# Optimization experiments

Measured on AMD Instinct MI355X. Metric: run time of the kernel, lower is better.

The kernel has to match this reference:

```python
import jax, jax.numpy as jnp
import numpy as np

E, L, D, H, S, B = 8, 12, 768, 12, 512, 32
DIMS = [12, 8, 8, 8, 8, 12]
RANKS = [1, 8, 8, 8, 8, 8, 1]
ALPHA = 8.0


def setup_inputs() -> dict:
    key = jax.random.key(0)
    ks = iter(jax.random.split(key, 32))
    inp = {}
    inp['hidden_states'] = jax.random.normal(next(ks), (B, S, D), jnp.float32)
    inp['router_weights'] = jax.random.normal(next(ks), (D, E), jnp.float32)
    for pre in ('q', 'v'):
        for i in range(6):
            shp = (E, L, RANKS[i], DIMS[i], RANKS[i + 1])
            inp[f'{pre}_core{i}'] = jax.random.normal(next(ks), shp, jnp.float32) * 0.05
    for nm in ('Wq', 'Wk', 'Wv', 'Wo'):
        inp[nm] = jax.random.normal(next(ks), (L, D, D), jnp.float32) * 0.02
    for nm in ('bq', 'bk', 'bv', 'bo'):
        inp[nm] = jnp.zeros((L, D), jnp.float32)
    inp['ln_scale'] = jnp.ones((L, D), jnp.float32)
    inp['ln_bias'] = jnp.zeros((L, D), jnp.float32)
    return inp


def _layernorm(x, scale, bias, eps=1e-12):
    mu = x.mean(-1, keepdims=True)
    var = ((x - mu) ** 2).mean(-1, keepdims=True)
    return (x - mu) * jax.lax.rsqrt(var + eps) * scale + bias


def _tt_weights(cores):
    # cores[i]: [L, r_i, d_i, r_{i+1}]; chained TT contraction, vectorized over layers
    w = jnp.einsum('Lijk,Lklm,Lmno,Lopq,Lqrs,Lstu->Ljlnprt', *cores)
    return w.reshape(w.shape[0], D, D)  # [L, out, in] (matches torch weight.reshape)


def reference(hidden_states, router_weights,
              q_core0, q_core1, q_core2, q_core3, q_core4, q_core5,
              v_core0, v_core1, v_core2, v_core3, v_core4, v_core5,
              Wq, Wk, Wv, Wo, bq, bk, bv, bo, ln_scale, ln_bias):
    # routing: pool over sequence, softmax + argmax per sample
    pooled = hidden_states.mean(axis=1)                      # [B, D]
    probs = jax.nn.softmax(pooled @ router_weights, axis=-1)  # [B, E]
    idx = jnp.argmax(probs, axis=-1)                          # [B]
    e = idx[-1]
    qc = [c[e] for c in (q_core0, q_core1, q_core2, q_core3, q_core4, q_core5)]
    vc = [c[e] for c in (v_core0, v_core1, v_core2, v_core3, v_core4, v_core5)]
    Wq_a = Wq + ALPHA * _tt_weights(qc)  # [L, D, D]
    Wv_a = Wv + ALPHA * _tt_weights(vc)

    hd = D // H
    scale = 1.0 / jnp.sqrt(jnp.float32(hd))
    x = hidden_states
    for l in range(L):
        q = (x @ Wq_a[l].T + bq[l]).reshape(B, S, H, hd)
        k = (x @ Wk[l].T + bk[l]).reshape(B, S, H, hd)
        v = (x @ Wv_a[l].T + bv[l]).reshape(B, S, H, hd)
        scores = jnp.einsum('bqhd,bkhd->bhqk', q, k) * scale
        attn = jax.nn.softmax(scores, axis=-1)
        ctx = jnp.einsum('bhqk,bkhd->bqhd', attn, v).reshape(B, S, D)
        out = ctx @ Wo[l].T + bo[l]
        x = _layernorm(x + out, ln_scale[l], ln_bias[l])
    return x
```

## Files before the change

### kernel.cpp

```cpp
#include <hip/hip_runtime.h>
#include <hip/hip_bf16.h>
#include <stdint.h>

#define E_ 8
#define L_ 12
#define D_ 768
#define H_ 12
#define S_ 512
#define B_ 32
#define BS_ (B_*S_)

typedef __attribute__((ext_vector_type(4))) float floatx4;
typedef __attribute__((ext_vector_type(8))) __bf16 bf16x8;
typedef __attribute__((ext_vector_type(4))) __bf16 bf16x4;
typedef __attribute__((ext_vector_type(2))) unsigned uintx2;

__device__ __forceinline__ __bf16 f2bf(float f) {
  unsigned u = __builtin_bit_cast(unsigned, f);
  u += 0x7fffu + ((u >> 16) & 1u);
  unsigned short h = (unsigned short)(u >> 16);
  return __builtin_bit_cast(__bf16, h);
}

__device__ __forceinline__ unsigned cvtpk_bf16(float lo, float hi) {
  unsigned r;
  asm("v_cvt_pk_bf16_f32 %0, %1, %2" : "=v"(r) : "v"(lo), "v"(hi));
  return r;
}

__device__ __forceinline__ float fexp2(float x) {
#if __has_builtin(__builtin_amdgcn_exp2f)
  return __builtin_amdgcn_exp2f(x);
#else
  return exp2f(x);
#endif
}

__device__ __forceinline__ void async16(const void* g, void* l) {
  __builtin_amdgcn_global_load_lds((__attribute__((address_space(1))) void*)g,
                                   (__attribute__((address_space(3))) void*)l,
                                   16, 0, 0);
}

__global__ void routing_pool_kernel(const float* __restrict__ hidden,
                                    float* __restrict__ partial) {
  const int blk = blockIdx.x;
  const int tid = threadIdx.x;
  const float* base = hidden + (size_t)(B_-1)*S_*D_ + (size_t)blk*8*D_;
  float acc[3] = {0.f, 0.f, 0.f};
  for (int s = 0; s < 8; ++s) {
#pragma unroll
    for (int i = 0; i < 3; ++i)
      acc[i] += base[(size_t)s*D_ + tid + i*256];
  }
#pragma unroll
  for (int i = 0; i < 3; ++i) partial[(size_t)blk*D_ + tid + i*256] = acc[i];
}

__global__ void routing_finish_kernel(const float* __restrict__ partial,
                                      const float* __restrict__ rw,
                                      int* __restrict__ e_out) {
  __shared__ float pooled[D_];
  __shared__ float logits[E_];
  int tid = threadIdx.x;
#pragma unroll
  for (int i = 0; i < 3; ++i) {
    int d = tid + i*256;
    float s = 0.f;
    for (int blk = 0; blk < 64; ++blk) s += partial[(size_t)blk*D_ + d];
    pooled[d] = s;
  }
  __syncthreads();
  if (tid < E_) {
    float s = 0.f;
    for (int d = 0; d < D_; ++d) s += pooled[d] * rw[d*E_ + tid];
    logits[tid] = s;
  }
  __syncthreads();
  if (tid == 0) {
    int best = 0; float bvv = logits[0];
    for (int e = 1; e < E_; ++e) if (logits[e] > bvv) { bvv = logits[e]; best = e; }
    e_out[0] = best;
  }
}

__global__ void convert_bf16_kernel(const float* __restrict__ src, __bf16* __restrict__ dst) {
  size_t i = ((size_t)blockIdx.x*256 + threadIdx.x)*8;
  __bf16 r[8];
#pragma unroll
  for (int j = 0; j < 8; ++j) r[j] = f2bf(src[i+j]);
  *(bf16x8*)(dst + i) = *(bf16x8*)r;
}

__global__ void convert_wk_kernel(const float* __restrict__ wk, __bf16* __restrict__ wqkv) {
  size_t i = ((size_t)blockIdx.x*256 + threadIdx.x)*8;
  int l = (int)(i / (D_*D_));
  int rem = (int)(i % (D_*D_));
  int n = rem / D_, k = rem % D_;
  __bf16 r[8];
#pragma unroll
  for (int j = 0; j < 8; ++j) r[j] = f2bf(wk[i+j]);
  *(bf16x8*)(wqkv + (size_t)l*2304*D_ + (size_t)(768+n)*D_ + k) = *(bf16x8*)r;
}

__global__ void tt_prep_kernel(
    const float* __restrict__ qc0, const float* __restrict__ qc1, const float* __restrict__ qc2,
    const float* __restrict__ qc3, const float* __restrict__ qc4, const float* __restrict__ qc5,
    const float* __restrict__ vc0, const float* __restrict__ vc1, const float* __restrict__ vc2,
    const float* __restrict__ vc3, const float* __restrict__ vc4, const float* __restrict__ vc5,
    const float* __restrict__ Wq, const float* __restrict__ Wv,
    const int* __restrict__ e_idx, __bf16* __restrict__ wqkv) {
  const int l = blockIdx.x;
  const int pre = blockIdx.y;
  const int z = blockIdx.z;
  const int tid = threadIdx.x;
  const int e = e_idx[0];
  const float* c0 = (pre ? vc0 : qc0) + (size_t)(e*L_ + l)*96;
  const float* c1 = (pre ? vc1 : qc1) + (size_t)(e*L_ + l)*512;
  const float* c2 = (pre ? vc2 : qc2) + (size_t)(e*L_ + l)*512;
  const float* c3 = (pre ? vc3 : qc3) + (size_t)(e*L_ + l)*512;
  const float* c4 = (pre ? vc4 : qc4) + (size_t)(e*L_ + l)*512;
  const float* c5 = (pre ? vc5 : qc5) + (size_t)(e*L_ + l)*96;
  __shared__ float M1[768];
  __shared__ float R2[768];
  __shared__ float M2[6144];
  __shared__ float Rm[6144];
  for (int idx = tid; idx < 768; idx += 256) {
    int j = idx >> 6, rem = idx & 63, l2 = rem >> 3, m = rem & 7;
    float s = 0.f;
    for (int k = 0; k < 8; ++k) s += c0[j*8 + k] * c1[k*64 + l2*8 + m];
    M1[idx] = s;
    int qq = idx / 96, rem2 = idx % 96, rr = rem2 / 12, t = rem2 % 12;
    float s2 = 0.f;
    for (int si = 0; si < 8; ++si) s2 += c4[qq*64 + rr*8 + si] * c5[si*12 + t];
    R2[idx] = s2;
  }
  __syncthreads();
  for (int idx = tid; idx < 6144; idx += 256) {
    int o = idx & 7, n = (idx >> 3) & 7, jl = idx >> 6;
    float s = 0.f;
    for (int m = 0; m < 8; ++m) s += M1[jl*8 + m] * c2[m*64 + n*8 + o];
    M2[idx] = s;
    int o2 = idx / 768, inp = idx % 768, p = inp / 96, rt = inp % 96;
    float s2 = 0.f;
    for (int qq = 0; qq < 8; ++qq) s2 += c3[o2*64 + p*8 + qq] * R2[qq*96 + rt];
    Rm[idx] = s2;
  }
  __syncthreads();
  const float* Wbase = (pre ? Wv : Wq) + (size_t)l*D_*D_;
  __bf16* dst = wqkv + (size_t)l*2304*D_ + (pre ? (size_t)1536*D_ : 0);
  for (int g = tid; g < 48*96; g += 256) {
    const int outr = z*48 + (g / 96);
    const int inp0 = (g % 96) * 8;
    float m2r[8];
#pragma unroll
    for (int o = 0; o < 8; ++o) m2r[o] = M2[outr*8 + o];
    float acc[8];
#pragma unroll
    for (int u = 0; u < 8; ++u) acc[u] = 0.f;
#pragma unroll
    for (int o = 0; o < 8; ++o) {
      float4 r0 = *(const float4*)&Rm[o*768 + inp0];
      float4 r1 = *(const float4*)&Rm[o*768 + inp0 + 4];
      acc[0] += m2r[o]*r0.x; acc[1] += m2r[o]*r0.y;
      acc[2] += m2r[o]*r0.z; acc[3] += m2r[o]*r0.w;
      acc[4] += m2r[o]*r1.x; acc[5] += m2r[o]*r1.y;
      acc[6] += m2r[o]*r1.z; acc[7] += m2r[o]*r1.w;
    }
    const float* wb = Wbase + (size_t)outr*768 + inp0;
    float4 w0 = *(const float4*)wb;
    float4 w1 = *(const float4*)(wb + 4);
    __bf16 r[8];
    r[0] = f2bf(w0.x + 8.f*acc[0]); r[1] = f2bf(w0.y + 8.f*acc[1]);
    r[2] = f2bf(w0.z + 8.f*acc[2]); r[3] = f2bf(w0.w + 8.f*acc[3]);
    r[4] = f2bf(w1.x + 8.f*acc[4]); r[5] = f2bf(w1.y + 8.f*acc[5]);
    r[6] = f2bf(w1.z + 8.f*acc[6]); r[7] = f2bf(w1.w + 8.f*acc[7]);
    *(bf16x8*)(dst + (size_t)outr*768 + inp0) = *(bf16x8*)r;
  }
}

#define SLOT_BYTES 28672
template<bool SPLITV>
__global__ __launch_bounds__(512, 2) void gemm_bt(
    const __bf16* __restrict__ A, const __bf16* __restrict__ Bw,
    const float* __restrict__ bq, const float* __restrict__ bk, const float* __restrict__ bvp,
    __bf16* __restrict__ outb, __bf16* __restrict__ vtout, int Nw) {
  __shared__ __align__(16) char lds[4*SLOT_BYTES];
  const int tid = threadIdx.x;
  const int w = tid >> 6, lane = tid & 63;
  const int quad = lane >> 4, l16 = lane & 15;
  const int wm = w >> 2, wn = w & 3;
  const size_t mblk = (size_t)blockIdx.y * 256;
  const size_t nblk = (size_t)blockIdx.x * 192;
  const __bf16* Ag = A + mblk * 768;
  const __bf16* Bg = Bw + nblk * 768;

  int a_goff[2], a_loff[2];
#pragma unroll
  for (int i = 0; i < 2; ++i) {
    int line = w*16 + i*8 + (lane >> 3);
    int s8 = (lane & 7) ^ (line & 7);
    int row = 2*line + (s8 >> 2);
    a_goff[i] = row*768 + (s8 & 3)*8;
    a_loff[i] = (w*16 + i*8)*128;
  }
  int b_goff[2], b_loff[2];
#pragma unroll
  for (int i = 0; i < 2; ++i) {
    int bl0 = (w < 4) ? (w*16 + i*8) : (64 + (w-4)*8);
    int line = bl0 + (lane >> 3);
    int s8 = (lane & 7) ^ (line & 7);
    int row = 2*line + (s8 >> 2);
    b_goff[i] = row*768 + (s8 & 3)*8;
    b_loff[i] = 16384 + bl0*128;
  }

  int a_foff[8], b_foff[3];
#pragma unroll
  for (int mf = 0; mf < 8; ++mf) {
    int r = wm*128 + mf*16 + l16;
    int line = r >> 1, s8 = (r & 1)*4 + quad, ph = s8 ^ (line & 7);
    a_foff[mf] = line*128 + ph*16;
  }
#pragma unroll
  for (int nf = 0; nf < 3; ++nf) {
    int r = wn*48 + nf*16 + l16;
    int line = r >> 1, s8 = (r & 1)*4 + quad, ph = s8 ^ (line & 7);
    b_foff[nf] = 16384 + line*128 + ph*16;
  }

  floatx4 acc[8][3];
#pragma unroll
  for (int mf = 0; mf < 8; ++mf)
#pragma unroll
    for (int nf = 0; nf < 3; ++nf) acc[mf][nf] = {0.f,0.f,0.f,0.f};

  auto STAGE = [&](int t) {
    const __bf16* Ab = Ag + t*32;
    const __bf16* Bb = Bg + t*32;
    char* ls = lds + (t & 3)*SLOT_BYTES;
    async16(Ab + a_goff[0], ls + a_loff[0]);
    async16(Ab + a_goff[1], ls + a_loff[1]);
    if (w < 4) {
      async16(Bb + b_goff[0], ls + b_loff[0]);
      async16(Bb + b_goff[1], ls + b_loff[1]);
    } else {
      async16(Bb + b_goff[0], ls + b_loff[0]);
    }
  };

  bf16x8 af[8], bfr[3];
  auto LOAD1 = [&](int u) {
    const char* ls = lds + (u & 3)*SLOT_BYTES;
#pragma unroll
    for (int nf = 0; nf < 3; ++nf) bfr[nf] = *(const bf16x8*)(ls + b_foff[nf]);
#pragma unroll
    for (int mf = 0; mf < 4; ++mf) af[mf] = *(const bf16x8*)(ls + a_foff[mf]);
  };
  auto LOAD2 = [&](int u) {
    const char* ls = lds + (u & 3)*SLOT_BYTES;
#pragma unroll
    for (int mf = 4; mf < 8; ++mf) af[mf] = *(const bf16x8*)(ls + a_foff[mf]);
  };
  auto MM = [&](int mf0) {
    __builtin_amdgcn_s_setprio(1);
#pragma unroll
    for (int mf = mf0; mf < mf0 + 4; ++mf)
#pragma unroll
      for (int nf = 0; nf < 3; ++nf)
        acc[mf][nf] = __builtin_amdgcn_mfma_f32_16x16x32_bf16(af[mf], bfr[nf], acc[mf][nf], 0, 0, 0);
    __builtin_amdgcn_s_setprio(0);
  };
  auto BAR = [&]() {
    __builtin_amdgcn_s_barrier();
    __builtin_amdgcn_sched_barrier(0);
  };

  STAGE(0); STAGE(1); STAGE(2);
  if (w < 4) asm volatile("s_waitcnt vmcnt(8)" ::: "memory");
  else       asm volatile("s_waitcnt vmcnt(6)" ::: "memory");
  BAR();

  for (int u = 0; u < 21; ++u) {
    LOAD1(u);
    BAR();
    MM(0);
    LOAD2(u);
    STAGE(u + 3);
    if (w < 4) asm volatile("s_waitcnt vmcnt(8)" ::: "memory");
    else       asm volatile("s_waitcnt vmcnt(6)" ::: "memory");
    BAR();
    MM(4);
  }
  LOAD1(21);
  BAR();
  MM(0);
  LOAD2(21);
  if (w < 4) asm volatile("s_waitcnt vmcnt(4)" ::: "memory");
  else       asm volatile("s_waitcnt vmcnt(3)" ::: "memory");
  BAR();
  MM(4);
  LOAD1(22);
  BAR();
  MM(0);
  LOAD2(22);
  asm volatile("s_waitcnt vmcnt(0)" ::: "memory");
  BAR();
  MM(4);
  LOAD1(23);
  BAR();
  MM(0);
  LOAD2(23);
  BAR();
  MM(4);

  if (SPLITV && blockIdx.x >= 8) {
#pragma unroll
    for (int nf = 0; nf < 3; ++nf) {
      const int vcol = (int)nblk - 1536 + wn*48 + nf*16 + l16;
      const int h = vcol >> 6, d = vcol & 63;
      const float bval = bvp[vcol];
#pragma unroll
      for (int mf = 0; mf < 8; ++mf) {
        const int mrow = (int)mblk + wm*128 + mf*16 + quad*4;
        const int b = mrow >> 9, s = mrow & 511;
        __bf16 pr[4];
#pragma unroll
        for (int r = 0; r < 4; ++r) pr[r] = f2bf(acc[mf][nf][r] + bval);
        *(bf16x4*)(vtout + (size_t)((b*H_ + h)*64 + d)*S_ + s) = *(bf16x4*)pr;
      }
    }
    return;
  }
  const float* bias = bq;
  if (SPLITV) bias = (blockIdx.x < 4) ? bq : bk;
  float bval[3]; int ncol[3];
#pragma unroll
  for (int nf = 0; nf < 3; ++nf) {
    ncol[nf] = (int)nblk + wn*48 + nf*16 + l16;
    int bc = ncol[nf]; if (bc >= 768) bc -= 768;
    bval[nf] = bias[bc];
  }
#pragma unroll
  for (int mf = 0; mf < 8; ++mf) {
#pragma unroll
    for (int nf = 0; nf < 3; ++nf) {
#pragma unroll
      for (int r = 0; r < 4; ++r) {
        const int mrow = (int)mblk + wm*128 + mf*16 + quad*4 + r;
        outb[(size_t)mrow*Nw + ncol[nf]] = f2bf(acc[mf][nf][r] + bval[nf]);
      }
    }
  }
}

#define PSTR 72
__global__ __launch_bounds__(256, 4) void flash_kernel(const __bf16* __restrict__ qkv,
                                                       const __bf16* __restrict__ vt,
                                                       __bf16* __restrict__ ctx) {
  __shared__ __align__(16) __bf16 Ks[64*PSTR];
  __shared__ __align__(16) __bf16 Vts[64*PSTR];
  __shared__ __align__(16) __bf16 Ps[64*PSTR];
  const int tid = threadIdx.x;
  const int w = tid >> 6, lane = tid & 63;
  const int quad = lane >> 4, l16 = lane & 15;
  const int n = blockIdx.x;
  const int bh = (n >> 6)*8 + (n & 7);
  const int q0 = ((n >> 3) & 7) * 64;
  const int b = bh / H_, h = bh % H_;
  const float SCL = 0.125f * 1.44269504f;

  const int row0 = tid >> 3,         seg0 = tid & 7;
  const int row1 = (256 + tid) >> 3, seg1 = tid & 7;

  bf16x8 ka[2], va[2], kb[2], vb[2];
  ka[0] = *(const bf16x8*)(qkv + (size_t)(b*S_ + row0)*2304 + 768 + h*64 + seg0*8);
  va[0] = *(const bf16x8*)(vt  + (size_t)(bh*64 + row0)*S_ + seg0*8);
  ka[1] = *(const bf16x8*)(qkv + (size_t)(b*S_ + row1)*2304 + 768 + h*64 + seg1*8);
  va[1] = *(const bf16x8*)(vt  + (size_t)(bh*64 + row1)*S_ + seg1*8);

  bf16x8 qf0, qf1;
  {
    const __bf16* qrow = qkv + (size_t)(b*S_ + q0 + w*16 + l16)*2304 + h*64 + quad*8;
    qf0 = *(const bf16x8*)qrow;
    qf1 = *(const bf16x8*)(qrow + 32);
  }

  const __bf16* kp0 = qkv + (size_t)(b*S_ + 64 + row0)*2304 + 768 + h*64 + seg0*8;
  const __bf16* kp1 = qkv + (size_t)(b*S_ + 64 + row1)*2304 + 768 + h*64 + seg1*8;
  const __bf16* vp0 = vt  + (size_t)(bh*64 + row0)*S_ + 64 + seg0*8;
  const __bf16* vp1 = vt  + (size_t)(bh*64 + row1)*S_ + 64 + seg1*8;

  floatx4 acc_o[4];
#pragma unroll
  for (int jd = 0; jd < 4; ++jd) acc_o[jd] = {0.f,0.f,0.f,0.f};
  float m_prev = -__builtin_inff();
  float l_part = 0.f;

  auto STEP = [&](bf16x8* ck, bf16x8* cv, bf16x8* nk, bf16x8* nv, bool pf) {
    asm volatile("s_waitcnt lgkmcnt(0)" ::: "memory");
    __builtin_amdgcn_s_barrier();
    __builtin_amdgcn_sched_barrier(0);
    *(bf16x8*)&Ks[row0*PSTR + seg0*8]  = ck[0];
    *(bf16x8*)&Vts[row0*PSTR + seg0*8] = cv[0];
    *(bf16x8*)&Ks[row1*PSTR + seg1*8]  = ck[1];
    *(bf16x8*)&Vts[row1*PSTR + seg1*8] = cv[1];
    if (pf) {
      nk[0] = *(const bf16x8*)kp0; kp0 += 64*2304;
      nv[0] = *(const bf16x8*)vp0; vp0 += 64;
      nk[1] = *(const bf16x8*)kp1; kp1 += 64*2304;
      nv[1] = *(const bf16x8*)vp1; vp1 += 64;
    }
    asm volatile("s_waitcnt lgkmcnt(0)" ::: "memory");
    __builtin_amdgcn_s_barrier();
    __builtin_amdgcn_sched_barrier(0);

    floatx4 sacc[4];
#pragma unroll
    for (int i = 0; i < 4; ++i) sacc[i] = {0.f,0.f,0.f,0.f};
    __builtin_amdgcn_s_setprio(1);
#pragma unroll
    for (int kk = 0; kk < 64; kk += 32) {
      bf16x8 bq_ = kk ? qf1 : qf0;
#pragma unroll
      for (int i = 0; i < 4; ++i) {
        bf16x8 ak = *(const bf16x8*)&Ks[(i*16 + l16)*PSTR + kk + quad*8];
        sacc[i] = __builtin_amdgcn_mfma_f32_16x16x32_bf16(ak, bq_, sacc[i], 0, 0, 0);
      }
    }
    __builtin_amdgcn_s_setprio(0);
#pragma unroll
    for (int i = 0; i < 4; ++i)
#pragma unroll
      for (int r = 0; r < 4; ++r) sacc[i][r] *= SCL;
    float mloc = sacc[0][0];
#pragma unroll
    for (int i = 0; i < 4; ++i)
#pragma unroll
      for (int r = 0; r < 4; ++r) mloc = fmaxf(mloc, sacc[i][r]);
    mloc = fmaxf(mloc, __shfl_xor(mloc, 16));
    mloc = fmaxf(mloc, __shfl_xor(mloc, 32));
    const bool resc = !__all(mloc <= m_prev + 10.f);
    float mnew = m_prev;
    if (resc) mnew = fmaxf(m_prev, mloc);
    float rsum = 0.f;
#pragma unroll
    for (int i = 0; i < 4; ++i) {
      float p0 = fexp2(sacc[i][0] - mnew);
      float p1 = fexp2(sacc[i][1] - mnew);
      float p2 = fexp2(sacc[i][2] - mnew);
      float p3 = fexp2(sacc[i][3] - mnew);
      rsum += (p0 + p1) + (p2 + p3);
      uintx2 pk = { cvtpk_bf16(p0, p1), cvtpk_bf16(p2, p3) };
      *(uintx2*)&Ps[(w*16 + l16)*PSTR + i*16 + quad*4] = pk;
    }
    if (resc) {
      float alpha = fexp2(m_prev - mnew);
      m_prev = mnew;
      l_part *= alpha;
      float ab[4];
#pragma unroll
      for (int r = 0; r < 4; ++r) ab[r] = __shfl(alpha, quad*4 + r);
#pragma unroll
      for (int jd = 0; jd < 4; ++jd)
#pragma unroll
        for (int r = 0; r < 4; ++r) acc_o[jd][r] *= ab[r];
    }
    l_part += rsum;
#pragma unroll
    for (int kk = 0; kk < 64; kk += 32) {
      bf16x8 ap = *(const bf16x8*)&Ps[(w*16 + l16)*PSTR + kk + quad*8];
      __builtin_amdgcn_s_setprio(1);
#pragma unroll
      for (int jd = 0; jd < 4; ++jd) {
        bf16x8 bv_ = *(const bf16x8*)&Vts[(jd*16 + l16)*PSTR + kk + quad*8];
        acc_o[jd] = __builtin_amdgcn_mfma_f32_16x16x32_bf16(ap, bv_, acc_o[jd], 0, 0, 0);
      }
      __builtin_amdgcn_s_setprio(0);
    }
  };

#pragma unroll
  for (int kt2 = 0; kt2 < 8; kt2 += 2) {
    STEP(ka, va, kb, vb, true);
    STEP(kb, vb, ka, va, kt2 + 1 < 7);
  }

  float l_tot = l_part;
  l_tot += __shfl_xor(l_tot, 16);
  l_tot += __shfl_xor(l_tot, 32);
  float lb[4];
#pragma unroll
  for (int r = 0; r < 4; ++r) lb[r] = 1.f / __shfl(l_tot, quad*4 + r);
#pragma unroll
  for (int jd = 0; jd < 4; ++jd) {
    const int d = jd*16 + l16;
#pragma unroll
    for (int r = 0; r < 4; ++r) {
      const int q = q0 + w*16 + quad*4 + r;
      ctx[(size_t)(b*S_ + q)*D_ + h*64 + d] = f2bf(acc_o[jd][r] * lb[r]);
    }
  }
}

template<bool FIRST, bool LAST>
__global__ __launch_bounds__(256) void ln_kernel(const float* __restrict__ residf,
                                                 __bf16* xb,
                                                 const __bf16* __restrict__ proj,
                                                 const float* __restrict__ gamma,
                                                 const float* __restrict__ beta,
                                                 float* __restrict__ xoutf) {
  const int tid = threadIdx.x;
  const int w = tid >> 6, lane = tid & 63;
  const int row = blockIdx.x*4 + w;
  const size_t base = (size_t)row * D_;
  const int c0 = lane*8;
  const bool has2 = lane < 32;
  const int c1 = 512 + lane*8;

  float v0[8], v1[8];
  {
    bf16x8 p0 = *(const bf16x8*)(proj + base + c0);
    if (FIRST) {
      float4 a = *(const float4*)(residf + base + c0);
      float4 bq4 = *(const float4*)(residf + base + c0 + 4);
      v0[0]=a.x+(float)p0[0]; v0[1]=a.y+(float)p0[1]; v0[2]=a.z+(float)p0[2]; v0[3]=a.w+(float)p0[3];
      v0[4]=bq4.x+(float)p0[4]; v0[5]=bq4.y+(float)p0[5]; v0[6]=bq4.z+(float)p0[6]; v0[7]=bq4.w+(float)p0[7];
    } else {
      bf16x8 r0 = *(const bf16x8*)(xb + base + c0);
#pragma unroll
      for (int j = 0; j < 8; ++j) v0[j] = (float)r0[j] + (float)p0[j];
    }
    if (has2) {
      bf16x8 p1 = *(const bf16x8*)(proj + base + c1);
      if (FIRST) {
        float4 a = *(const float4*)(residf + base + c1);
        float4 bq4 = *(const float4*)(residf + base + c1 + 4);
        v1[0]=a.x+(float)p1[0]; v1[1]=a.y+(float)p1[1]; v1[2]=a.z+(float)p1[2]; v1[3]=a.w+(float)p1[3];
        v1[4]=bq4.x+(float)p1[4]; v1[5]=bq4.y+(float)p1[5]; v1[6]=bq4.z+(float)p1[6]; v1[7]=bq4.w+(float)p1[7];
      } else {
        bf16x8 r1 = *(const bf16x8*)(xb + base + c1);
#pragma unroll
        for (int j = 0; j < 8; ++j) v1[j] = (float)r1[j] + (float)p1[j];
      }
    } else {
#pragma unroll
      for (int j = 0; j < 8; ++j) v1[j] = 0.f;
    }
  }
  float s = 0.f;
#pragma unroll
  for (int j = 0; j < 8; ++j) s += v0[j] + v1[j];
#pragma unroll
  for (int off = 32; off; off >>= 1) s += __shfl_xor(s, off);
  const float mu = s * (1.f/768.f);
  float q = 0.f;
#pragma unroll
  for (int j = 0; j < 8; ++j) { float d0 = v0[j]-mu; q += d0*d0; }
  if (has2) {
#pragma unroll
    for (int j = 0; j < 8; ++j) { float d1 = v1[j]-mu; q += d1*d1; }
  }
#pragma unroll
  for (int off = 32; off; off >>= 1) q += __shfl_xor(q, off);
  const float rs = rsqrtf(q * (1.f/768.f) + 1e-12f);

  {
    float4 g0 = *(const float4*)(gamma + c0);
    float4 g1 = *(const float4*)(gamma + c0 + 4);
    float4 b0 = *(const float4*)(beta + c0);
    float4 b1 = *(const float4*)(beta + c0 + 4);
    float o[8];
    o[0]=(v0[0]-mu)*rs*g0.x+b0.x; o[1]=(v0[1]-mu)*rs*g0.y+b0.y;
    o[2]=(v0[2]-mu)*rs*g0.z+b0.z; o[3]=(v0[3]-mu)*rs*g0.w+b0.w;
    o[4]=(v0[4]-mu)*rs*g1.x+b1.x; o[5]=(v0[5]-mu)*rs*g1.y+b1.y;
    o[6]=(v0[6]-mu)*rs*g1.z+b1.z; o[7]=(v0[7]-mu)*rs*g1.w+b1.w;
    if (LAST) {
      *(float4*)(xoutf + base + c0)     = {o[0],o[1],o[2],o[3]};
      *(float4*)(xoutf + base + c0 + 4) = {o[4],o[5],o[6],o[7]};
    } else {
      __bf16 ob[8];
#pragma unroll
      for (int j = 0; j < 8; ++j) ob[j] = f2bf(o[j]);
      *(bf16x8*)(xb + base + c0) = *(bf16x8*)ob;
    }
  }
  if (has2) {
    float4 g0 = *(const float4*)(gamma + c1);
    float4 g1 = *(const float4*)(gamma + c1 + 4);
    float4 b0 = *(const float4*)(beta + c1);
    float4 b1 = *(const float4*)(beta + c1 + 4);
    float o[8];
    o[0]=(v1[0]-mu)*rs*g0.x+b0.x; o[1]=(v1[1]-mu)*rs*g0.y+b0.y;
    o[2]=(v1[2]-mu)*rs*g0.z+b0.z; o[3]=(v1[3]-mu)*rs*g0.w+b0.w;
    o[4]=(v1[4]-mu)*rs*g1.x+b1.x; o[5]=(v1[5]-mu)*rs*g1.y+b1.y;
    o[6]=(v1[6]-mu)*rs*g1.z+b1.z; o[7]=(v1[7]-mu)*rs*g1.w+b1.w;
    if (LAST) {
      *(float4*)(xoutf + base + c1)     = {o[0],o[1],o[2],o[3]};
      *(float4*)(xoutf + base + c1 + 4) = {o[4],o[5],o[6],o[7]};
    } else {
      __bf16 ob[8];
#pragma unroll
      for (int j = 0; j < 8; ++j) ob[j] = f2bf(o[j]);
      *(bf16x8*)(xb + base + c1) = *(bf16x8*)ob;
    }
  }
}

extern "C" void kernel_launch(void* const* d_in, const int* in_sizes, int n_in,
                              void* d_out, int out_size, void* d_ws, size_t ws_size,
                              hipStream_t stream) {
  const float* hidden = (const float*)d_in[0];
  const float* router = (const float*)d_in[1];
  const float* qc[6]; const float* vc[6];
  for (int i = 0; i < 6; ++i) qc[i] = (const float*)d_in[2+i];
  for (int i = 0; i < 6; ++i) vc[i] = (const float*)d_in[8+i];
  const float* Wq = (const float*)d_in[14];
  const float* Wk = (const float*)d_in[15];
  const float* Wv = (const float*)d_in[16];
  const float* Wo = (const float*)d_in[17];
  const float* bq = (const float*)d_in[18];
  const float* bk = (const float*)d_in[19];
  const float* bv = (const float*)d_in[20];
  const float* bo = (const float*)d_in[21];
  const float* lns = (const float*)d_in[22];
  const float* lnb = (const float*)d_in[23];
  float* out = (float*)d_out;

  char* ws = (char*)d_ws;
  size_t off = 0;
  auto alloc = [&](size_t bytes) -> void* {
    off = (off + 255) & ~(size_t)255;
    void* p = ws + off; off += bytes; return p;
  };
  int*    e_idx = (int*)   alloc(4);
  float*  rpart = (float*) alloc((size_t)64*D_*4);
  __bf16* xbf   = (__bf16*)alloc((size_t)BS_*D_*2);
  __bf16* qkv   = (__bf16*)alloc((size_t)BS_*2304*2);
  __bf16* vt    = (__bf16*)alloc((size_t)B_*H_*64*S_*2);
  __bf16* ctx   = (__bf16*)alloc((size_t)BS_*D_*2);
  __bf16* projb = (__bf16*)alloc((size_t)BS_*D_*2);
  __bf16* wqkv  = (__bf16*)alloc((size_t)L_*2304*D_*2);
  __bf16* wobf  = (__bf16*)alloc((size_t)L_*D_*D_*2);
  (void)ws_size; (void)in_sizes; (void)n_in; (void)out_size;

  routing_pool_kernel<<<64, 256, 0, stream>>>(hidden, rpart);
  routing_finish_kernel<<<1, 256, 0, stream>>>(rpart, router, e_idx);
  convert_bf16_kernel<<<(BS_*D_)/2048, 256, 0, stream>>>(hidden, xbf);
  tt_prep_kernel<<<dim3(L_, 2, 16), 256, 0, stream>>>(qc[0],qc[1],qc[2],qc[3],qc[4],qc[5],
                                                      vc[0],vc[1],vc[2],vc[3],vc[4],vc[5],
                                                      Wq, Wv, e_idx, wqkv);
  convert_wk_kernel<<<(L_*D_*D_)/2048, 256, 0, stream>>>(Wk, wqkv);
  convert_bf16_kernel<<<(L_*D_*D_)/2048, 256, 0, stream>>>(Wo, wobf);

  for (int l = 0; l < L_; ++l) {
    gemm_bt<true><<<dim3(12,64), 512, 0, stream>>>(xbf, wqkv + (size_t)l*2304*D_,
        bq + l*D_, bk + l*D_, bv + l*D_, qkv, vt, 2304);
    flash_kernel<<<3072, 256, 0, stream>>>(qkv, vt, ctx);
    gemm_bt<false><<<dim3(4,64), 512, 0, stream>>>(ctx, wobf + (size_t)l*D_*D_,
        bo + l*D_, nullptr, nullptr, projb, nullptr, 768);
    if (l == 0)
      ln_kernel<true,false><<<BS_/4, 256, 0, stream>>>(hidden, xbf, projb,
          lns + l*D_, lnb + l*D_, nullptr);
    else if (l == L_-1)
      ln_kernel<false,true><<<BS_/4, 256, 0, stream>>>(nullptr, xbf, projb,
          lns + l*D_, lnb + l*D_, out);
    else
      ln_kernel<false,false><<<BS_/4, 256, 0, stream>>>(nullptr, xbf, projb,
          lns + l*D_, lnb + l*D_, nullptr);
  }
}
```

Baseline: 2.254 ms.

## Shrink GEMM block tile to 128x192 with four waves and more blocks

Changes the bf16 GEMM from 256x192 tiles with 8 waves to 128x192 tiles with 4 waves. Each wave still computes 128x48, and the grid doubles along M. Global-to-LDS staging is redistributed so each wave issues five async copies, and the vmcnt waits are updated to match. LDS per block shrinks, but each block reuses the B tile over fewer rows, so total B traffic rises. In exchange there are more blocks to spread across the CUs (e.g. 512 instead of 256 for the output projection).

```diff
diff --git a/kernel.cpp b/kernel.cpp
--- a/kernel.cpp
+++ b/kernel.cpp
@@ -179,9 +179,9 @@
   }
 }
 
-#define SLOT_BYTES 28672
+#define SLOT_BYTES 20480
 template<bool SPLITV>
-__global__ __launch_bounds__(512, 2) void gemm_bt(
+__global__ __launch_bounds__(256, 2) void gemm_bt(
     const __bf16* __restrict__ A, const __bf16* __restrict__ Bw,
     const float* __restrict__ bq, const float* __restrict__ bk, const float* __restrict__ bvp,
     __bf16* __restrict__ outb, __bf16* __restrict__ vtout, int Nw) {
@@ -189,44 +189,37 @@
   const int tid = threadIdx.x;
   const int w = tid >> 6, lane = tid & 63;
   const int quad = lane >> 4, l16 = lane & 15;
-  const int wm = w >> 2, wn = w & 3;
-  const size_t mblk = (size_t)blockIdx.y * 256;
+  const size_t mblk = (size_t)blockIdx.y * 128;
   const size_t nblk = (size_t)blockIdx.x * 192;
   const __bf16* Ag = A + mblk * 768;
   const __bf16* Bg = Bw + nblk * 768;
 
-  int a_goff[2], a_loff[2];
-#pragma unroll
-  for (int i = 0; i < 2; ++i) {
-    int line = w*16 + i*8 + (lane >> 3);
+  const __bf16* gbase[5];
+  int loff[5];
+#pragma unroll
+  for (int i = 0; i < 5; ++i) {
+    int c = w*5 + i;
+    bool isA = c < 8;
+    int lb = isA ? c*8 : (c-8)*8;
+    int line = lb + (lane >> 3);
     int s8 = (lane & 7) ^ (line & 7);
     int row = 2*line + (s8 >> 2);
-    a_goff[i] = row*768 + (s8 & 3)*8;
-    a_loff[i] = (w*16 + i*8)*128;
-  }
-  int b_goff[2], b_loff[2];
-#pragma unroll
-  for (int i = 0; i < 2; ++i) {
-    int bl0 = (w < 4) ? (w*16 + i*8) : (64 + (w-4)*8);
-    int line = bl0 + (lane >> 3);
-    int s8 = (lane & 7) ^ (line & 7);
-    int row = 2*line + (s8 >> 2);
-    b_goff[i] = row*768 + (s8 & 3)*8;
-    b_loff[i] = 16384 + bl0*128;
+    gbase[i] = (isA ? Ag : Bg) + row*768 + (s8 & 3)*8;
+    loff[i] = (isA ? 0 : 8192) + lb*128;
   }
 
   int a_foff[8], b_foff[3];
 #pragma unroll
   for (int mf = 0; mf < 8; ++mf) {
-    int r = wm*128 + mf*16 + l16;
+    int r = mf*16 + l16;
     int line = r >> 1, s8 = (r & 1)*4 + quad, ph = s8 ^ (line & 7);
     a_foff[mf] = line*128 + ph*16;
   }
 #pragma unroll
   for (int nf = 0; nf < 3; ++nf) {
-    int r = wn*48 + nf*16 + l16;
+    int r = w*48 + nf*16 + l16;
     int line = r >> 1, s8 = (r & 1)*4 + quad, ph = s8 ^ (line & 7);
-    b_foff[nf] = 16384 + line*128 + ph*16;
+    b_foff[nf] = 8192 + line*128 + ph*16;
   }
 
   floatx4 acc[8][3];
@@ -236,17 +229,9 @@
     for (int nf = 0; nf < 3; ++nf) acc[mf][nf] = {0.f,0.f,0.f,0.f};
 
   auto STAGE = [&](int t) {
-    const __bf16* Ab = Ag + t*32;
-    const __bf16* Bb = Bg + t*32;
     char* ls = lds + (t & 3)*SLOT_BYTES;
-    async16(Ab + a_goff[0], ls + a_loff[0]);
-    async16(Ab + a_goff[1], ls + a_loff[1]);
-    if (w < 4) {
-      async16(Bb + b_goff[0], ls + b_loff[0]);
-      async16(Bb + b_goff[1], ls + b_loff[1]);
-    } else {
-      async16(Bb + b_goff[0], ls + b_loff[0]);
-    }
+#pragma unroll
+    for (int i = 0; i < 5; ++i) async16(gbase[i] + t*32, ls + loff[i]);
   };
 
   bf16x8 af[8], bfr[3];
@@ -277,8 +262,7 @@
   };
 
   STAGE(0); STAGE(1); STAGE(2);
-  if (w < 4) asm volatile("s_waitcnt vmcnt(8)" ::: "memory");
-  else       asm volatile("s_waitcnt vmcnt(6)" ::: "memory");
+  asm volatile("s_waitcnt vmcnt(10)" ::: "memory");
   BAR();
 
   for (int u = 0; u < 21; ++u) {
@@ -287,8 +271,7 @@
     MM(0);
     LOAD2(u);
     STAGE(u + 3);
-    if (w < 4) asm volatile("s_waitcnt vmcnt(8)" ::: "memory");
-    else       asm volatile("s_waitcnt vmcnt(6)" ::: "memory");
+    asm volatile("s_waitcnt vmcnt(10)" ::: "memory");
     BAR();
     MM(4);
   }
@@ -296,8 +279,7 @@
   BAR();
   MM(0);
   LOAD2(21);
-  if (w < 4) asm volatile("s_waitcnt vmcnt(4)" ::: "memory");
-  else       asm volatile("s_waitcnt vmcnt(3)" ::: "memory");
+  asm volatile("s_waitcnt vmcnt(5)" ::: "memory");
   BAR();
   MM(4);
   LOAD1(22);
@@ -317,12 +299,12 @@
   if (SPLITV && blockIdx.x >= 8) {
 #pragma unroll
     for (int nf = 0; nf < 3; ++nf) {
-      const int vcol = (int)nblk - 1536 + wn*48 + nf*16 + l16;
+      const int vcol = (int)nblk - 1536 + w*48 + nf*16 + l16;
       const int h = vcol >> 6, d = vcol & 63;
       const float bval = bvp[vcol];
 #pragma unroll
       for (int mf = 0; mf < 8; ++mf) {
-        const int mrow = (int)mblk + wm*128 + mf*16 + quad*4;
+        const int mrow = (int)mblk + mf*16 + quad*4;
         const int b = mrow >> 9, s = mrow & 511;
         __bf16 pr[4];
 #pragma unroll
@@ -337,7 +319,7 @@
   float bval[3]; int ncol[3];
 #pragma unroll
   for (int nf = 0; nf < 3; ++nf) {
-    ncol[nf] = (int)nblk + wn*48 + nf*16 + l16;
+    ncol[nf] = (int)nblk + w*48 + nf*16 + l16;
     int bc = ncol[nf]; if (bc >= 768) bc -= 768;
     bval[nf] = bias[bc];
   }
@@ -347,7 +329,7 @@
     for (int nf = 0; nf < 3; ++nf) {
 #pragma unroll
       for (int r = 0; r < 4; ++r) {
-        const int mrow = (int)mblk + wm*128 + mf*16 + quad*4 + r;
+        const int mrow = (int)mblk + mf*16 + quad*4 + r;
         outb[(size_t)mrow*Nw + ncol[nf]] = f2bf(acc[mf][nf][r] + bval[nf]);
       }
     }
@@ -654,10 +636,10 @@
   convert_bf16_kernel<<<(L_*D_*D_)/2048, 256, 0, stream>>>(Wo, wobf);
 
   for (int l = 0; l < L_; ++l) {
-    gemm_bt<true><<<dim3(12,64), 512, 0, stream>>>(xbf, wqkv + (size_t)l*2304*D_,
+    gemm_bt<true><<<dim3(12,128), 256, 0, stream>>>(xbf, wqkv + (size_t)l*2304*D_,
         bq + l*D_, bk + l*D_, bv + l*D_, qkv, vt, 2304);
     flash_kernel<<<3072, 256, 0, stream>>>(qkv, vt, ctx);
-    gemm_bt<false><<<dim3(4,64), 512, 0, stream>>>(ctx, wobf + (size_t)l*D_*D_,
+    gemm_bt<false><<<dim3(4,128), 256, 0, stream>>>(ctx, wobf + (size_t)l*D_*D_,
         bo + l*D_, nullptr, nullptr, projb, nullptr, 768);
     if (l == 0)
       ln_kernel<true,false><<<BS_/4, 256, 0, stream>>>(hidden, xbf, projb,
```

After: 2.252 ms. About the same (-0.1%).
